# Kernel tuning notes

Hardware: AMD Instinct MI355X
Metric: run time of the kernel (lower is better)

The kernel has to match this reference:

```python
import jax, jax.numpy as jnp
import numpy as np

N_NODES = 100000
N_EDGES = 800000
N_GRAPHS = 2000
IN_DIM = 64
HID = 32
HEADS = 4
NEG_SLOPE = 0.2


def _glorot(key, shape, fan_in, fan_out):
    lim = np.sqrt(6.0 / (fan_in + fan_out)).astype(np.float32)
    return jax.random.uniform(key, shape, jnp.float32, -lim, lim)


def setup_inputs() -> dict:
    key = jax.random.key(0)
    ks = jax.random.split(key, 16)
    x = jax.random.normal(ks[0], (N_NODES, IN_DIM), jnp.float32)
    edge_index = jax.random.randint(ks[1], (2, N_EDGES), 0, N_NODES, jnp.int64)
    batch = jnp.sort(jax.random.randint(ks[2], (N_NODES,), 0, N_GRAPHS, jnp.int64))
    HF = HEADS * HID
    params = {
        "W1": _glorot(ks[3], (IN_DIM, HF), IN_DIM, HF),
        "a1_src": _glorot(ks[4], (HEADS, HID), HID, HID),
        "a1_dst": _glorot(ks[5], (HEADS, HID), HID, HID),
        "b1": jnp.zeros((HF,), jnp.float32),
        "W2": _glorot(ks[6], (HF, HF), HF, HF),
        "a2_src": _glorot(ks[7], (HEADS, HID), HID, HID),
        "a2_dst": _glorot(ks[8], (HEADS, HID), HID, HID),
        "b2": jnp.zeros((HF,), jnp.float32),
        "W3": _glorot(ks[9], (HF, HF), HF, HF),
        "a3_src": _glorot(ks[10], (HEADS, HID), HID, HID),
        "a3_dst": _glorot(ks[11], (HEADS, HID), HID, HID),
        "b3": jnp.zeros((HID,), jnp.float32),  # concat=False -> bias over out dim
        "Wm1": _glorot(ks[12], (HID, 64), HID, 64),
        "bm1": jnp.zeros((64,), jnp.float32),
        "Wm2": _glorot(ks[13], (64, 1), 64, 1),
        "bm2": jnp.zeros((1,), jnp.float32),
    }
    return {"x": x, "edge_index": edge_index, "batch": batch, **params}


def gat_conv(x, src, dst, W, a_src, a_dst, bias, concat):
    # PyG GATConv (eval mode, self-loops already in src/dst).
    N = x.shape[0]
    H, F = a_src.shape
    h = (x @ W).reshape(N, H, F)                     # [N,H,F]
    as_n = jnp.sum(h * a_src, axis=-1)               # [N,H] per-node src term
    ad_n = jnp.sum(h * a_dst, axis=-1)               # [N,H] per-node dst term
    logits = jax.nn.leaky_relu(as_n[src] + ad_n[dst], NEG_SLOPE)  # [Et,H]
    # segment softmax over incoming edges of each dst node
    m = jax.ops.segment_max(logits, dst, num_segments=N)          # [N,H]
    e = jnp.exp(logits - m[dst])
    denom = jax.ops.segment_sum(e, dst, num_segments=N)           # [N,H], >0 via self-loops
    alpha = e / denom[dst]                                        # [Et,H]
    msg = h[src] * alpha[:, :, None]                              # [Et,H,F]
    out = jax.ops.segment_sum(msg, dst, num_segments=N)           # [N,H,F]
    out = out.reshape(N, H * F) if concat else out.mean(axis=1)
    return out + bias


def reference(x, edge_index, batch, W1, a1_src, a1_dst, b1, W2, a2_src, a2_dst, b2,
              W3, a3_src, a3_dst, b3, Wm1, bm1, Wm2, bm2):
    N = x.shape[0]
    loops = jnp.arange(N, dtype=edge_index.dtype)
    src = jnp.concatenate([edge_index[0], loops])
    dst = jnp.concatenate([edge_index[1], loops])

    h = jax.nn.elu(gat_conv(x, src, dst, W1, a1_src, a1_dst, b1, True))
    h = jax.nn.elu(gat_conv(h, src, dst, W2, a2_src, a2_dst, b2, True))
    h = jax.nn.elu(gat_conv(h, src, dst, W3, a3_src, a3_dst, b3, False))

    # global_mean_pool over batch ids
    sums = jax.ops.segment_sum(h, batch, num_segments=N_GRAPHS)           # [G,HID]
    cnts = jax.ops.segment_sum(jnp.ones((N,), h.dtype), batch, num_segments=N_GRAPHS)
    pooled = sums / jnp.maximum(cnts, 1.0)[:, None]

    z = jax.nn.relu(pooled @ Wm1 + bm1)
    out = (z @ Wm2 + bm2).squeeze(-1)                                     # [G]
    return out
```

## Files before the change

kernel.cpp:

```cpp
#include <hip/hip_runtime.h>

#define N_NODES  100000
#define N_EDGES  800000
#define ET       900000
#define N_GRAPHS 2000
#define IN_DIM   64
#define HID      32
#define HEADS    4
#define HF       128
#define NEG_SLOPE 0.2f

typedef __attribute__((ext_vector_type(8))) short bf16x8;
typedef __attribute__((ext_vector_type(4))) float f32x4;

__device__ __forceinline__ float lrelu(float x) { return x > 0.f ? x : NEG_SLOPE * x; }
__device__ __forceinline__ float elu_f(float x) { return x > 0.f ? x : expm1f(x); }
__device__ __forceinline__ unsigned fenc(float f) {
  unsigned u = __float_as_uint(f);
  return (u & 0x80000000u) ? ~u : (u | 0x80000000u);
}
__device__ __forceinline__ float fdec(unsigned e) {
  return __uint_as_float((e & 0x80000000u) ? (e ^ 0x80000000u) : ~e);
}
__device__ __forceinline__ unsigned short bf16_rne(float f) {
  unsigned u = __float_as_uint(f);
  unsigned r = (u + 0x7fffu + ((u >> 16) & 1u)) >> 16;
  return (unsigned short)r;
}

__global__ void k_count(const int* __restrict__ ei, int* __restrict__ deg) {
  int e = blockIdx.x * 256 + threadIdx.x;
  if (e >= ET) return;
  int d = (e < N_EDGES) ? ei[N_EDGES + e] : (e - N_EDGES);
  atomicAdd(&deg[d], 1);
}

__global__ void k_scan1(const int* __restrict__ deg, int* __restrict__ rs, int* __restrict__ bsums) {
  __shared__ int sd[256];
  int t = threadIdx.x;
  int i = blockIdx.x * 256 + t;
  int v = (i < N_NODES) ? deg[i] : 0;
  sd[t] = v; __syncthreads();
  for (int s = 1; s < 256; s <<= 1) {
    int tmp = (t >= s) ? sd[t - s] : 0; __syncthreads();
    sd[t] += tmp; __syncthreads();
  }
  if (i < N_NODES) rs[i] = sd[t] - v;
  if (t == 255) bsums[blockIdx.x] = sd[255];
}

__global__ void k_scan2(int* __restrict__ bsums, int nb) {
  __shared__ int sd[512];
  int t = threadIdx.x;
  int v = (t < nb) ? bsums[t] : 0;
  sd[t] = v; __syncthreads();
  for (int s = 1; s < 512; s <<= 1) {
    int tmp = (t >= s) ? sd[t - s] : 0; __syncthreads();
    sd[t] += tmp; __syncthreads();
  }
  if (t < nb) bsums[t] = sd[t] - v;
}

__global__ void k_scan3(int* __restrict__ rs, const int* __restrict__ bsums) {
  int i = blockIdx.x * 256 + threadIdx.x;
  if (i < N_NODES) rs[i] += bsums[blockIdx.x];
  if (i == 0) rs[N_NODES] = ET;
}

__global__ void k_fill(const int* __restrict__ ei, const int* __restrict__ rs,
                       int* __restrict__ fill, int* __restrict__ csr_src) {
  int e = blockIdx.x * 256 + threadIdx.x;
  if (e >= ET) return;
  int s, d;
  if (e < N_EDGES) { s = ei[e]; d = ei[N_EDGES + e]; }
  else             { s = e - N_EDGES; d = s; }
  int pos = atomicAdd(&fill[d], 1);
  csr_src[rs[d] + pos] = s;
}

template<int K>
__global__ void k_prep(const float* __restrict__ W, const float* __restrict__ as_,
                       const float* __restrict__ ad_,
                       unsigned short* __restrict__ Bh, unsigned short* __restrict__ Bl) {
  int idx = blockIdx.x * 256 + threadIdx.x;
  if (idx >= K * 144) return;
  int k = idx / 144, c = idx % 144;
  float v = 0.f;
  if (c < 128) {
    v = W[k * 128 + c];
  } else if (c < 136) {
    int h = (c - 128) & 3;
    const float* av = (c < 132) ? as_ : ad_;
    float s = 0.f;
    for (int f = 0; f < HID; ++f) s += W[k * 128 + h * HID + f] * av[h * HID + f];
    v = s;
  }
  unsigned short hi = bf16_rne(v);
  float hf = __uint_as_float((unsigned)hi << 16);
  unsigned short lo = bf16_rne(v - hf);
  size_t dst = ((size_t)(k >> 3) * 144 + c) * 8 + (k & 7);
  Bh[dst] = hi;
  Bl[dst] = lo;
}

template<int K>
__global__ void __launch_bounds__(256, 2) k_gemm_attn(
    const float* __restrict__ X,
    const unsigned short* __restrict__ Bh, const unsigned short* __restrict__ Bl,
    float* __restrict__ H, float* __restrict__ AS, float* __restrict__ AD,
    unsigned* __restrict__ M4) {
  __shared__ short sBh[K * 144];
  __shared__ short sBl[K * 144];
  const int t = threadIdx.x;
  const int l = t & 63;
  const int w = t >> 6;
  const int m = l & 15;
  const int g = l >> 4;
  const int row0 = blockIdx.x * 128 + w * 32;

  for (int i = t; i < K * 18; i += 256) {
    ((bf16x8*)sBh)[i] = ((const bf16x8*)Bh)[i];
    ((bf16x8*)sBl)[i] = ((const bf16x8*)Bl)[i];
  }
  __syncthreads();

  f32x4 acc[2][9];
#pragma unroll
  for (int a = 0; a < 2; ++a)
#pragma unroll
    for (int b = 0; b < 9; ++b) acc[a][b] = (f32x4){0.f, 0.f, 0.f, 0.f};

  for (int kb = 0; kb < K; kb += 32) {
    bf16x8 ahi[2], alo[2];
#pragma unroll
    for (int tr = 0; tr < 2; ++tr) {
      int row = row0 + tr * 16 + m;
      float4 xa = make_float4(0.f, 0.f, 0.f, 0.f);
      float4 xb = make_float4(0.f, 0.f, 0.f, 0.f);
      if (row < N_NODES) {
        const float4* xp = (const float4*)&X[(size_t)row * K + kb + g * 8];
        xa = xp[0]; xb = xp[1];
      }
      float xv[8] = {xa.x, xa.y, xa.z, xa.w, xb.x, xb.y, xb.z, xb.w};
#pragma unroll
      for (int j = 0; j < 8; ++j) {
        unsigned short h = bf16_rne(xv[j]);
        float hf = __uint_as_float((unsigned)h << 16);
        unsigned short lo2 = bf16_rne(xv[j] - hf);
        ahi[tr][j] = (short)h;
        alo[tr][j] = (short)lo2;
      }
    }
    const int kfl = ((kb >> 3) + g) * 144;
#pragma unroll
    for (int tc = 0; tc < 9; ++tc) {
      bf16x8 bh = *(const bf16x8*)(sBh + (kfl + tc * 16 + m) * 8);
      bf16x8 bl = *(const bf16x8*)(sBl + (kfl + tc * 16 + m) * 8);
#pragma unroll
      for (int tr = 0; tr < 2; ++tr) {
        acc[tr][tc] = __builtin_amdgcn_mfma_f32_16x16x32_bf16(ahi[tr], bh, acc[tr][tc], 0, 0, 0);
        acc[tr][tc] = __builtin_amdgcn_mfma_f32_16x16x32_bf16(ahi[tr], bl, acc[tr][tc], 0, 0, 0);
        acc[tr][tc] = __builtin_amdgcn_mfma_f32_16x16x32_bf16(alo[tr], bh, acc[tr][tc], 0, 0, 0);
      }
    }
  }

  float vmax = -3.4e38f;
#pragma unroll
  for (int tr = 0; tr < 2; ++tr) {
    int rbase = row0 + tr * 16 + g * 4;
#pragma unroll
    for (int tc = 0; tc < 8; ++tc) {
      int col = tc * 16 + m;
#pragma unroll
      for (int e = 0; e < 4; ++e) {
        int row = rbase + e;
        if (row < N_NODES) H[(size_t)row * HF + col] = acc[tr][tc][e];
      }
    }
#pragma unroll
    for (int e = 0; e < 4; ++e) {
      int row = rbase + e;
      float v = acc[tr][8][e];
      if (row < N_NODES) {
        if (m < 4) AS[row * HEADS + m] = v;
        else if (m < 8) AD[row * HEADS + (m - 4)] = v;
      }
      vmax = fmaxf(vmax, v);
    }
  }
  vmax = fmaxf(vmax, __shfl_xor(vmax, 16));
  vmax = fmaxf(vmax, __shfl_xor(vmax, 32));
  if (g == 0 && m < 4) atomicMax(&M4[m], fenc(vmax));
}

template<bool CONCAT>
__global__ void __launch_bounds__(256) k_aggregate(
    const int* __restrict__ rs, const int* __restrict__ csr_src,
    const float* __restrict__ H, const float* __restrict__ AS,
    const float* __restrict__ AD, const unsigned* __restrict__ M4,
    const float* __restrict__ bias, float* __restrict__ OUT) {
  int n = blockIdx.x * 8 + (threadIdx.x >> 5);
  if (n >= N_NODES) return;
  int sl = threadIdx.x & 31;
  int c = sl * 4;
  int head = sl >> 3;
  int b = rs[n], e = rs[n + 1];

  float ad = AD[4 * n + head];
  float m = lrelu(fdec(M4[head]) + ad);

  float ax = 0.f, ay = 0.f, az = 0.f, aw = 0.f, den = 0.f;
  int jj = b;
  for (; jj + 3 < e; jj += 4) {
    int s0 = csr_src[jj];
    int s1 = csr_src[jj + 1];
    int s2 = csr_src[jj + 2];
    int s3 = csr_src[jj + 3];
    float e0 = __expf(lrelu(AS[4 * s0 + head] + ad) - m);
    float e1 = __expf(lrelu(AS[4 * s1 + head] + ad) - m);
    float e2 = __expf(lrelu(AS[4 * s2 + head] + ad) - m);
    float e3 = __expf(lrelu(AS[4 * s3 + head] + ad) - m);
    float4 h0 = *(const float4*)&H[(size_t)s0 * HF + c];
    float4 h1 = *(const float4*)&H[(size_t)s1 * HF + c];
    float4 h2 = *(const float4*)&H[(size_t)s2 * HF + c];
    float4 h3 = *(const float4*)&H[(size_t)s3 * HF + c];
    ax += h0.x * e0 + h1.x * e1 + h2.x * e2 + h3.x * e3;
    ay += h0.y * e0 + h1.y * e1 + h2.y * e2 + h3.y * e3;
    az += h0.z * e0 + h1.z * e1 + h2.z * e2 + h3.z * e3;
    aw += h0.w * e0 + h1.w * e1 + h2.w * e2 + h3.w * e3;
    den += (e0 + e1) + (e2 + e3);
  }
  for (; jj < e; ++jj) {
    int s0 = csr_src[jj];
    float e0 = __expf(lrelu(AS[4 * s0 + head] + ad) - m);
    float4 h0 = *(const float4*)&H[(size_t)s0 * HF + c];
    ax += h0.x * e0; ay += h0.y * e0; az += h0.z * e0; aw += h0.w * e0;
    den += e0;
  }

  float invd = 1.f / den;
  if (CONCAT) {
    float4 o;
    o.x = elu_f(ax * invd + bias[c]);
    o.y = elu_f(ay * invd + bias[c + 1]);
    o.z = elu_f(az * invd + bias[c + 2]);
    o.w = elu_f(aw * invd + bias[c + 3]);
    *(float4*)&OUT[(size_t)n * HF + c] = o;
  } else {
    ax *= invd; ay *= invd; az *= invd; aw *= invd;
    ax += __shfl_xor(ax, 8);  ay += __shfl_xor(ay, 8);
    az += __shfl_xor(az, 8);  aw += __shfl_xor(aw, 8);
    ax += __shfl_xor(ax, 16); ay += __shfl_xor(ay, 16);
    az += __shfl_xor(az, 16); aw += __shfl_xor(aw, 16);
    if (sl < 8) {
      int cc = sl * 4;
      float4 o;
      o.x = elu_f(0.25f * ax + bias[cc]);
      o.y = elu_f(0.25f * ay + bias[cc + 1]);
      o.z = elu_f(0.25f * az + bias[cc + 2]);
      o.w = elu_f(0.25f * aw + bias[cc + 3]);
      *(float4*)&OUT[(size_t)n * HID + cc] = o;
    }
  }
}

__global__ void __launch_bounds__(64) k_pool_mlp(
    const int* __restrict__ batch, const float* __restrict__ H3,
    const float* __restrict__ Wm1, const float* __restrict__ bm1,
    const float* __restrict__ Wm2, const float* __restrict__ bm2,
    float* __restrict__ OUT) {
  int g = blockIdx.x;
  int t = threadIdx.x;
  __shared__ float pooled[HID];
  int lo = 0, hi = N_NODES;
  while (lo < hi) { int mid = (lo + hi) >> 1; if (batch[mid] < g) lo = mid + 1; else hi = mid; }
  int start = lo;
  hi = N_NODES;
  while (lo < hi) { int mid = (lo + hi) >> 1; if (batch[mid] < g + 1) lo = mid + 1; else hi = mid; }
  int end = lo;
  if (t < HID) {
    float s = 0.f;
    for (int n = start; n < end; ++n) s += H3[(size_t)n * HID + t];
    float cnt = (float)(end - start);
    pooled[t] = s / fmaxf(cnt, 1.f);
  }
  __syncthreads();
  float z = bm1[t];
#pragma unroll
  for (int f = 0; f < HID; ++f) z += pooled[f] * Wm1[f * 64 + t];
  z = fmaxf(z, 0.f);
  float p = z * Wm2[t];
  for (int off = 32; off > 0; off >>= 1) p += __shfl_down(p, off);
  if (t == 0) OUT[g] = p + bm2[0];
}

extern "C" void kernel_launch(void* const* d_in, const int* in_sizes, int n_in,
                              void* d_out, int out_size, void* d_ws, size_t ws_size,
                              hipStream_t stream) {
  const float* x    = (const float*)d_in[0];
  const int*   ei   = (const int*)d_in[1];
  const int*   batch= (const int*)d_in[2];
  const float* W1   = (const float*)d_in[3];
  const float* a1s  = (const float*)d_in[4];
  const float* a1d  = (const float*)d_in[5];
  const float* b1   = (const float*)d_in[6];
  const float* W2   = (const float*)d_in[7];
  const float* a2s  = (const float*)d_in[8];
  const float* a2d  = (const float*)d_in[9];
  const float* b2   = (const float*)d_in[10];
  const float* W3   = (const float*)d_in[11];
  const float* a3s  = (const float*)d_in[12];
  const float* a3d  = (const float*)d_in[13];
  const float* b3   = (const float*)d_in[14];
  const float* Wm1  = (const float*)d_in[15];
  const float* bm1  = (const float*)d_in[16];
  const float* Wm2  = (const float*)d_in[17];
  const float* bm2  = (const float*)d_in[18];
  float* out = (float*)d_out;

  char* p = (char*)d_ws;
  auto take = [&](size_t bytes) { char* r = p; p += (bytes + 255) & ~(size_t)255; return r; };
  float*          bufA = (float*)take((size_t)N_NODES * HF * 4);
  float*          bufB = (float*)take((size_t)N_NODES * HF * 4);
  float*          AS   = (float*)take((size_t)N_NODES * HEADS * 4);
  float*          AD   = (float*)take((size_t)N_NODES * HEADS * 4);
  unsigned*       M4   = (unsigned*)take(3 * 4 * 4);
  int*            deg  = (int*)take((size_t)N_NODES * 4);
  int*            rs   = (int*)take((size_t)(N_NODES + 1) * 4);
  int*            csr  = (int*)take((size_t)ET * 4);
  int*            bsums= (int*)take((size_t)512 * 4);
  unsigned short* Wh1  = (unsigned short*)take((size_t)IN_DIM * 144 * 2);
  unsigned short* Wl1  = (unsigned short*)take((size_t)IN_DIM * 144 * 2);
  unsigned short* Wh2  = (unsigned short*)take((size_t)HF * 144 * 2);
  unsigned short* Wl2  = (unsigned short*)take((size_t)HF * 144 * 2);
  unsigned short* Wh3  = (unsigned short*)take((size_t)HF * 144 * 2);
  unsigned short* Wl3  = (unsigned short*)take((size_t)HF * 144 * 2);

  unsigned* M4a = M4;
  unsigned* M4b = M4 + 4;
  unsigned* M4c = M4 + 8;

  const int nb_scan = (N_NODES + 255) / 256;

  k_prep<IN_DIM><<<(IN_DIM * 144 + 255) / 256, 256, 0, stream>>>(W1, a1s, a1d, Wh1, Wl1);
  k_prep<HF><<<(HF * 144 + 255) / 256, 256, 0, stream>>>(W2, a2s, a2d, Wh2, Wl2);
  k_prep<HF><<<(HF * 144 + 255) / 256, 256, 0, stream>>>(W3, a3s, a3d, Wh3, Wl3);

  hipMemsetAsync(deg, 0, (size_t)N_NODES * 4, stream);
  hipMemsetAsync(M4, 0, 48, stream);
  k_count<<<(ET + 255) / 256, 256, 0, stream>>>(ei, deg);
  k_scan1<<<nb_scan, 256, 0, stream>>>(deg, rs, bsums);
  k_scan2<<<1, 512, 0, stream>>>(bsums, nb_scan);
  k_scan3<<<nb_scan, 256, 0, stream>>>(rs, bsums);
  hipMemsetAsync(deg, 0, (size_t)N_NODES * 4, stream);
  k_fill<<<(ET + 255) / 256, 256, 0, stream>>>(ei, rs, deg, csr);

  const int gb = (N_NODES + 127) / 128;
  const int ab = (N_NODES + 7) / 8;

  k_gemm_attn<IN_DIM><<<gb, 256, 0, stream>>>(x, Wh1, Wl1, bufA, AS, AD, M4a);
  k_aggregate<true><<<ab, 256, 0, stream>>>(rs, csr, bufA, AS, AD, M4a, b1, bufB);
  k_gemm_attn<HF><<<gb, 256, 0, stream>>>(bufB, Wh2, Wl2, bufA, AS, AD, M4b);
  k_aggregate<true><<<ab, 256, 0, stream>>>(rs, csr, bufA, AS, AD, M4b, b2, bufB);
  k_gemm_attn<HF><<<gb, 256, 0, stream>>>(bufB, Wh3, Wl3, bufA, AS, AD, M4c);
  k_aggregate<false><<<ab, 256, 0, stream>>>(rs, csr, bufA, AS, AD, M4c, b3, bufB);
  k_pool_mlp<<<N_GRAPHS, 64, 0, stream>>>(batch, bufB, Wm1, bm1, Wm2, bm2, out);
}
```

Baseline: 520.8 us.

## Restructure GEMM-attention kernel: 16 rows per wave, chunked LDS weights, prefetch X

Each wave of the GEMM+attention-projection kernel now computes 16 rows instead of 32, and blocks cover 64 rows. The bf16 hi/lo weight copy in LDS is fixed at 64 K-rows and streamed in chunks, with barriers between chunks. The next X slice is loaded in registers before the current one is used. The aim is less register and LDS pressure so more blocks fit per CU (launch bounds raised to 4), and better hiding of X load latency. The cost is twice as many blocks, each reloading the B operand, plus extra syncs per chunk, and B fragments are no longer reused across two row tiles.

```diff
diff --git a/kernel.cpp b/kernel.cpp
--- a/kernel.cpp
+++ b/kernel.cpp
@@ -26,6 +26,16 @@
   unsigned u = __float_as_uint(f);
   unsigned r = (u + 0x7fffu + ((u >> 16) & 1u)) >> 16;
   return (unsigned short)r;
+}
+__device__ __forceinline__ void split8(const float4& a, const float4& b,
+                                       bf16x8& hi, bf16x8& lo) {
+  float xv[8] = {a.x, a.y, a.z, a.w, b.x, b.y, b.z, b.w};
+#pragma unroll
+  for (int j = 0; j < 8; ++j) {
+    unsigned short h = bf16_rne(xv[j]);
+    hi[j] = (short)h;
+    lo[j] = (short)bf16_rne(xv[j] - __uint_as_float((unsigned)h << 16));
+  }
 }
 
 __global__ void k_count(const int* __restrict__ ei, int* __restrict__ deg) {
@@ -104,90 +114,76 @@
 }
 
 template<int K>
-__global__ void __launch_bounds__(256, 2) k_gemm_attn(
+__global__ void __launch_bounds__(256, 4) k_gemm_attn(
     const float* __restrict__ X,
     const unsigned short* __restrict__ Bh, const unsigned short* __restrict__ Bl,
     float* __restrict__ H, float* __restrict__ AS, float* __restrict__ AD,
     unsigned* __restrict__ M4) {
-  __shared__ short sBh[K * 144];
-  __shared__ short sBl[K * 144];
+  __shared__ short sBh[64 * 144];
+  __shared__ short sBl[64 * 144];
   const int t = threadIdx.x;
   const int l = t & 63;
-  const int w = t >> 6;
   const int m = l & 15;
   const int g = l >> 4;
-  const int row0 = blockIdx.x * 128 + w * 32;
-
-  for (int i = t; i < K * 18; i += 256) {
-    ((bf16x8*)sBh)[i] = ((const bf16x8*)Bh)[i];
-    ((bf16x8*)sBl)[i] = ((const bf16x8*)Bl)[i];
-  }
-  __syncthreads();
-
-  f32x4 acc[2][9];
-#pragma unroll
-  for (int a = 0; a < 2; ++a)
-#pragma unroll
-    for (int b = 0; b < 9; ++b) acc[a][b] = (f32x4){0.f, 0.f, 0.f, 0.f};
-
-  for (int kb = 0; kb < K; kb += 32) {
-    bf16x8 ahi[2], alo[2];
-#pragma unroll
-    for (int tr = 0; tr < 2; ++tr) {
-      int row = row0 + tr * 16 + m;
-      float4 xa = make_float4(0.f, 0.f, 0.f, 0.f);
-      float4 xb = make_float4(0.f, 0.f, 0.f, 0.f);
-      if (row < N_NODES) {
-        const float4* xp = (const float4*)&X[(size_t)row * K + kb + g * 8];
-        xa = xp[0]; xb = xp[1];
+  const int row0 = blockIdx.x * 64 + (t >> 6) * 16;
+  const int arow = row0 + m;
+  const float* xrow = &X[(size_t)min(arow, N_NODES - 1) * K];
+
+  f32x4 acc[9];
+#pragma unroll
+  for (int b = 0; b < 9; ++b) acc[b] = (f32x4){0.f, 0.f, 0.f, 0.f};
+
+  float4 pxa = *(const float4*)&xrow[g * 8];
+  float4 pxb = *(const float4*)&xrow[g * 8 + 4];
+
+  for (int h = 0; h < K / 64; ++h) {
+    __syncthreads();
+    for (int i = t; i < 1152; i += 256) {
+      ((bf16x8*)sBh)[i] = ((const bf16x8*)Bh)[h * 1152 + i];
+      ((bf16x8*)sBl)[i] = ((const bf16x8*)Bl)[h * 1152 + i];
+    }
+    __syncthreads();
+#pragma unroll
+    for (int cc = 0; cc < 2; ++cc) {
+      bf16x8 ahi, alo;
+      split8(pxa, pxb, ahi, alo);
+      int kn = h * 64 + cc * 32 + 32;
+      if (kn < K) {
+        pxa = *(const float4*)&xrow[kn + g * 8];
+        pxb = *(const float4*)&xrow[kn + g * 8 + 4];
       }
-      float xv[8] = {xa.x, xa.y, xa.z, xa.w, xb.x, xb.y, xb.z, xb.w};
-#pragma unroll
-      for (int j = 0; j < 8; ++j) {
-        unsigned short h = bf16_rne(xv[j]);
-        float hf = __uint_as_float((unsigned)h << 16);
-        unsigned short lo2 = bf16_rne(xv[j] - hf);
-        ahi[tr][j] = (short)h;
-        alo[tr][j] = (short)lo2;
+      const int kfl = (cc * 4 + g) * 144;
+#pragma unroll
+      for (int tc = 0; tc < 9; ++tc) {
+        bf16x8 bh = *(const bf16x8*)(sBh + (kfl + tc * 16 + m) * 8);
+        bf16x8 bl = *(const bf16x8*)(sBl + (kfl + tc * 16 + m) * 8);
+        acc[tc] = __builtin_amdgcn_mfma_f32_16x16x32_bf16(ahi, bh, acc[tc], 0, 0, 0);
+        acc[tc] = __builtin_amdgcn_mfma_f32_16x16x32_bf16(ahi, bl, acc[tc], 0, 0, 0);
+        acc[tc] = __builtin_amdgcn_mfma_f32_16x16x32_bf16(alo, bh, acc[tc], 0, 0, 0);
       }
     }
-    const int kfl = ((kb >> 3) + g) * 144;
-#pragma unroll
-    for (int tc = 0; tc < 9; ++tc) {
-      bf16x8 bh = *(const bf16x8*)(sBh + (kfl + tc * 16 + m) * 8);
-      bf16x8 bl = *(const bf16x8*)(sBl + (kfl + tc * 16 + m) * 8);
-#pragma unroll
-      for (int tr = 0; tr < 2; ++tr) {
-        acc[tr][tc] = __builtin_amdgcn_mfma_f32_16x16x32_bf16(ahi[tr], bh, acc[tr][tc], 0, 0, 0);
-        acc[tr][tc] = __builtin_amdgcn_mfma_f32_16x16x32_bf16(ahi[tr], bl, acc[tr][tc], 0, 0, 0);
-        acc[tr][tc] = __builtin_amdgcn_mfma_f32_16x16x32_bf16(alo[tr], bh, acc[tr][tc], 0, 0, 0);
-      }
-    }
-  }
-
+  }
+
+  const int rbase = row0 + g * 4;
   float vmax = -3.4e38f;
 #pragma unroll
-  for (int tr = 0; tr < 2; ++tr) {
-    int rbase = row0 + tr * 16 + g * 4;
-#pragma unroll
-    for (int tc = 0; tc < 8; ++tc) {
-      int col = tc * 16 + m;
-#pragma unroll
-      for (int e = 0; e < 4; ++e) {
-        int row = rbase + e;
-        if (row < N_NODES) H[(size_t)row * HF + col] = acc[tr][tc][e];
-      }
-    }
+  for (int tc = 0; tc < 8; ++tc) {
+    int col = tc * 16 + m;
 #pragma unroll
     for (int e = 0; e < 4; ++e) {
-      int row = rbase + e;
-      float v = acc[tr][8][e];
-      if (row < N_NODES) {
-        if (m < 4) AS[row * HEADS + m] = v;
-        else if (m < 8) AD[row * HEADS + (m - 4)] = v;
-      }
-      vmax = fmaxf(vmax, v);
-    }
+      int r = rbase + e;
+      if (r < N_NODES) H[(size_t)r * HF + col] = acc[tc][e];
+    }
+  }
+#pragma unroll
+  for (int e = 0; e < 4; ++e) {
+    int r = rbase + e;
+    float v = acc[8][e];
+    if (r < N_NODES) {
+      if (m < 4) AS[r * HEADS + m] = v;
+      else if (m < 8) AD[r * HEADS + (m - 4)] = v;
+    }
+    vmax = fmaxf(vmax, v);
   }
   vmax = fmaxf(vmax, __shfl_xor(vmax, 16));
   vmax = fmaxf(vmax, __shfl_xor(vmax, 32));
@@ -356,7 +352,7 @@
   hipMemsetAsync(deg, 0, (size_t)N_NODES * 4, stream);
   k_fill<<<(ET + 255) / 256, 256, 0, stream>>>(ei, rs, deg, csr);
 
-  const int gb = (N_NODES + 127) / 128;
+  const int gb = (N_NODES + 63) / 64;
   const int ab = (N_NODES + 7) / 8;
 
   k_gemm_attn<IN_DIM><<<gb, 256, 0, stream>>>(x, Wh1, Wl1, bufA, AS, AD, M4a);
```

Measured after the change: 617.7 us. 18.6% more time.
